# Kernel tuning notes

Measured on AMD Instinct MI355X. Metric: run time of the kernel, lower is better.

Reference implementation:

```python
import jax, jax.numpy as jnp
import numpy as np

B, C, H, W = 2, 64, 256, 256
K, DG, PAD = 3, 8, 1
KK = K * K
CG = C // DG


def _conv(x, w, b):
    y = jax.lax.conv_general_dilated(x, w, (1, 1), [(PAD, PAD), (PAD, PAD)],
                                     dimension_numbers=('NCHW', 'OIHW', 'NCHW'))
    return y + b[None, :, None, None]


def _bilinear_one(img, y, x):
    # img: (CG, H, W); y, x: (KK, H, W) float sampling coords; zero-padded bilinear
    y0 = jnp.floor(y)
    x0 = jnp.floor(x)
    wy = y - y0
    wx = x - x0

    def tap(yi, xi, wgt):
        valid = (yi >= 0) & (yi < H) & (xi >= 0) & (xi < W)
        yc = jnp.clip(yi, 0, H - 1).astype(jnp.int32)
        xc = jnp.clip(xi, 0, W - 1).astype(jnp.int32)
        v = img[:, yc, xc]  # (CG, KK, H, W)
        return v * (wgt * valid)[None]

    return (tap(y0, x0, (1 - wy) * (1 - wx)) +
            tap(y0, x0 + 1, (1 - wy) * wx) +
            tap(y0 + 1, x0, wy * (1 - wx)) +
            tap(y0 + 1, x0 + 1, wy * wx))


_sample = jax.vmap(jax.vmap(_bilinear_one))  # over batch, then deform group


def setup_inputs() -> dict:
    key = jax.random.key(0)
    ks = jax.random.split(key, 7)
    n_off = 2 * KK * DG
    n_msk = KK * DG
    bound = 1.0 / np.sqrt(C * K * K)  # kaiming_uniform(a=sqrt(5)) bound
    return {
        'ref': jax.random.normal(ks[0], (B, C, H, W), jnp.float32),
        'neighbour': jax.random.normal(ks[1], (B, C, H, W), jnp.float32),
        'off_w': jax.random.normal(ks[2], (n_off, 2 * C, K, K), jnp.float32) * 0.01,
        'off_b': jnp.zeros((n_off,), jnp.float32),
        'mask_w': jax.random.normal(ks[3], (n_msk, 2 * C, K, K), jnp.float32) * 0.01,
        'mask_b': jnp.zeros((n_msk,), jnp.float32),
        'weight': jax.random.uniform(ks[4], (C, C, K, K), jnp.float32, -bound, bound),
        'bias': jnp.zeros((C,), jnp.float32),
    }


def reference(ref, neighbour, off_w, off_b, mask_w, mask_b, weight, bias):
    concat = jnp.concatenate([ref, neighbour], axis=1)            # (B, 2C, H, W)
    offset = _conv(concat, off_w, off_b)                          # (B, 2*DG*KK, H, W)
    mask = jax.nn.sigmoid(_conv(concat, mask_w, mask_b))          # (B, DG*KK, H, W)

    off = offset.reshape(B, DG, KK, 2, H, W)
    dy, dx = off[:, :, :, 0], off[:, :, :, 1]

    ki, kj = jnp.meshgrid(jnp.arange(K), jnp.arange(K), indexing='ij')
    ki = ki.reshape(KK).astype(jnp.float32)
    kj = kj.reshape(KK).astype(jnp.float32)
    base_y = jnp.arange(H, dtype=jnp.float32)[None, :, None] - PAD + ki[:, None, None]
    base_x = jnp.arange(W, dtype=jnp.float32)[None, None, :] - PAD + kj[:, None, None]
    ys = dy + base_y                                              # (B, DG, KK, H, W)
    xs = dx + base_x

    img_g = neighbour.reshape(B, DG, CG, H, W)
    sampled = _sample(img_g, ys, xs)                              # (B, DG, CG, KK, H, W)
    sampled = sampled * mask.reshape(B, DG, 1, KK, H, W)

    wr = weight.reshape(C, DG, CG, KK)
    out = jnp.einsum('bgckhw,ogck->bohw', sampled, wr)
    return out + bias[None, :, None, None]
```

## Files before the change

kernel.cpp:

```cpp
#include <hip/hip_runtime.h>
#include <hip/hip_fp16.h>
#include <cstdint>
#include <cstddef>

#define B_ 2
#define C_ 64
#define H_ 256
#define W_ 256
#define HW_ (H_*W_)
#define DG_ 8
#define CG_ 8
#define KK_ 9
#define NOFF_ 144
#define NMSK_ 72
#define NTOT_ 216
#define KRED_ 1152
#define XPH_ 258

typedef __bf16 bf16x8 __attribute__((ext_vector_type(8)));
typedef _Float16 half8 __attribute__((ext_vector_type(8)));
typedef short  short8 __attribute__((ext_vector_type(8)));
typedef float  f32x4  __attribute__((ext_vector_type(4)));

__device__ __forceinline__ short f2bf(float f) {
    union { float f; uint32_t u; } a; a.f = f;
    uint32_t u = a.u;
    uint32_t r = (u + 0x7fffu + ((u >> 16) & 1u)) >> 16;
    return (short)r;
}

typedef __attribute__((address_space(1))) const unsigned int g_u32;
typedef __attribute__((address_space(3))) unsigned int l_u32;
__device__ __forceinline__ void gl_lds16(const void* g, void* l) {
    __builtin_amdgcn_global_load_lds((g_u32*)g, (l_u32*)l, 16, 0, 0);
}

__global__ __launch_bounds__(256) void prep_all(
    const float* __restrict__ ref, const float* __restrict__ nbr,
    const float* __restrict__ off_w, const float* __restrict__ msk_w,
    const float* __restrict__ weight,
    short* __restrict__ xp, short* __restrict__ nbf,
    short* __restrict__ Bw, short* __restrict__ Bw3)
{
    const int bid = blockIdx.x;
    const int tid = threadIdx.x;

    if (bid < 2064) {
        const int by = bid >> 2;
        const int c4 = bid & 3;
        const int b  = by / XPH_;
        const int yi = by - b * XPH_;
        const int yg = yi - 1;
        const float* base = (c4 < 2 ? ref : nbr)
                            + ((size_t)b * 64 + (c4 & 1) * 32) * HW_;
        short* rowbase = xp + (((size_t)(b * 4 + c4) * XPH_ + yi) * XPH_) * 32;
        for (int xi = tid; xi < XPH_; xi += 256) {
            const int xg = xi - 1;
            const bool valid = ((unsigned)yg < H_) && ((unsigned)xg < W_);
            short* dst = rowbase + (size_t)xi * 32;
            const int sig = (xi >> 1) & 3;
            #pragma unroll
            for (int q = 0; q < 4; ++q) {
                float v[8];
                if (valid) {
                    const float* p = base + (size_t)(q * 8) * HW_
                                     + (size_t)yg * W_ + xg;
                    #pragma unroll
                    for (int j = 0; j < 8; ++j) v[j] = p[(size_t)j * HW_];
                } else {
                    #pragma unroll
                    for (int j = 0; j < 8; ++j) v[j] = 0.f;
                }
                short8 o;
                #pragma unroll
                for (int j = 0; j < 8; ++j) o[j] = f2bf(v[j]);
                *reinterpret_cast<short8*>(dst + ((q ^ sig) * 8)) = o;
                if (c4 >= 2 && valid) {
                    const int g = (c4 - 2) * 4 + q;
                    union { half8 h8; short8 s8; } u;
                    #pragma unroll
                    for (int j = 0; j < 8; ++j) u.h8[j] = (_Float16)v[j];
                    *reinterpret_cast<short8*>(
                        nbf + ((size_t)(b * 8 + g) * HW_
                               + (size_t)yg * W_ + xg) * 8) = u.s8;
                }
            }
        }
    } else if (bid < 3216) {
        int idx = (bid - 2064) * 256 + tid;
        int s    = idx >> 13;
        int rem  = idx & 8191;
        int n    = rem >> 5;
        int slot = (rem >> 3) & 3;
        int j    = rem & 7;
        int q    = slot ^ ((n >> 1) & 3);
        int c4   = s / 9;
        int tap  = s - c4 * 9;
        int ch   = c4 * 32 + q * 8 + j;
        float v = 0.f;
        if (n < NOFF_)      v = off_w[(size_t)n * KRED_ + ch * 9 + tap];
        else if (n < NTOT_) v = msk_w[(size_t)(n - NOFF_) * KRED_ + ch * 9 + tap];
        Bw[idx] = f2bf(v);
    } else {
        int idx = (bid - 3216) * 256 + tid;
        int kc   = idx >> 11;
        int rem  = idx & 2047;
        int n    = rem >> 5;
        int slot = (rem >> 3) & 3;
        int j    = rem & 7;
        int q    = slot ^ ((n >> 1) & 3);
        int k    = kc >> 1;
        int g    = ((kc & 1) << 2) + q;
        int ci   = g * 8 + j;
        union { _Float16 h; short s; } cv;
        cv.h = (_Float16)weight[((size_t)n * 64 + ci) * 9 + k];
        Bw3[idx] = cv.s;
    }
}

struct OffV { float dy, dx, mm; };
struct GathV { half8 c00, c01, c10, c11; float a00, a01, a10, a11; };

__global__ __launch_bounds__(512, 4) void fused_conv_apply(
    const short* __restrict__ xp, const short* __restrict__ Bw,
    const float* __restrict__ off_b, const float* __restrict__ msk_b,
    const short* __restrict__ nbf, const short* __restrict__ Bw3,
    const float* __restrict__ bias, float* __restrict__ out)
{
    __shared__ __align__(16) short AsBuf[2][4608];
    __shared__ __align__(16) short offmsk[NTOT_ * 128];

    const int tid  = threadIdx.x;
    const int lane = tid & 63;
    const int wid  = tid >> 6;
    const int wm   = wid & 1;
    const int wn   = wid >> 1;
    const int col     = lane & 15;
    const int quad    = lane >> 4;
    const int rowbase = quad * 4;

    const int bid = blockIdx.x;
    const int wg  = (bid & 7) * 128 + (bid >> 3);
    const int m0 = wg << 7;
    const int b  = m0 >> 16;
    const int h  = (m0 >> 8) & 255;
    const int w0 = m0 & 255;

    {
        int bOff[4];
        #pragma unroll
        for (int nt = 0; nt < 4; ++nt) {
            int n = wn * 64 + nt * 16 + col;
            bOff[nt] = (n * 4 + (quad ^ ((n >> 1) & 3))) * 8;
        }
        int pxv[4];
        #pragma unroll
        for (int mt = 0; mt < 4; ++mt) pxv[mt] = wm * 64 + mt * 16 + col;

        f32x4 acc[4][4];
        #pragma unroll
        for (int i = 0; i < 4; ++i)
            #pragma unroll
            for (int j = 0; j < 4; ++j) acc[i][j] = f32x4{0.f, 0.f, 0.f, 0.f};

        auto stageA = [&](int win, int bb) {
            const int c4s = win / 3;
            const int dys = win - c4s * 3;
            const short* sA = xp + (((size_t)(b * 4 + c4s) * XPH_ + (h + dys)) * XPH_
                                    + w0) * 32;
            char* dA = (char*)&AsBuf[bb][0];
            gl_lds16(sA + (size_t)tid * 8, dA + wid * 1024);
            if (tid < 32) gl_lds16(sA + (size_t)(512 + tid) * 8, dA + 8192);
        };

        stageA(0, 0);
        __syncthreads();

        #pragma unroll 1
        for (int win = 0; win < 12; ++win) {
            const int bb = win & 1;
            if (win < 11) stageA(win + 1, bb ^ 1);
            const short* AsC = &AsBuf[bb][0];

            #pragma unroll
            for (int dx = 0; dx < 3; ++dx) {
                const int s = win * 3 + dx;
                const short* bp = Bw + ((size_t)s << 13);

                bf16x8 bv[4];
                #pragma unroll
                for (int nt = 0; nt < 4; ++nt)
                    bv[nt] = *reinterpret_cast<const bf16x8*>(bp + bOff[nt]);

                bf16x8 af[4];
                #pragma unroll
                for (int mt = 0; mt < 4; ++mt) {
                    const int px = pxv[mt] + dx;
                    af[mt] = *reinterpret_cast<const bf16x8*>(
                        &AsC[(px * 4 + (quad ^ ((px >> 1) & 3))) * 8]);
                }

                __builtin_amdgcn_s_setprio(1);
                #pragma unroll
                for (int mt = 0; mt < 4; ++mt)
                    #pragma unroll
                    for (int nt = 0; nt < 4; ++nt)
                        acc[mt][nt] = __builtin_amdgcn_mfma_f32_16x16x32_bf16(
                            af[mt], bv[nt], acc[mt][nt], 0, 0, 0);
                __builtin_amdgcn_s_setprio(0);
            }
            __syncthreads();
        }

        #pragma unroll
        for (int mt = 0; mt < 4; ++mt) {
            const int p4 = wm * 64 + mt * 16 + rowbase;
            #pragma unroll
            for (int nt = 0; nt < 4; ++nt) {
                const int n = wn * 64 + nt * 16 + col;
                if (n >= NTOT_) continue;
                const bool is_off = (n < NOFF_);
                const float bia = is_off ? off_b[n] : msk_b[n - NOFF_];
                union { uint2 u; __half hx[4]; } pk;
                #pragma unroll
                for (int rr = 0; rr < 4; ++rr) {
                    float v = acc[mt][nt][rr] + bia;
                    if (!is_off) v = 1.f / (1.f + __expf(-v));
                    pk.hx[rr] = __float2half(v);
                }
                const int byt = n * 256 + ((2 * p4) ^ ((n & 7) << 4));
                *(uint2*)((char*)offmsk + byt) = pk.u;
            }
        }
    }
    __syncthreads();

    {
        const int p     = tid & 127;
        const int q     = tid >> 7;
        const int w     = w0 + p;
        const int slotW = q ^ ((p >> 1) & 3);

        auto ldsOff = [&](int n, int pp) -> float {
            const int byt = n * 256 + ((2 * pp) ^ ((n & 7) << 4));
            return __half2float(*reinterpret_cast<const __half*>(
                (const char*)offmsk + byt));
        };
        auto loadOffs = [&](int kc) -> OffV {
            const int k = kc >> 1;
            const int g = ((kc & 1) << 2) + q;
            OffV o;
            o.dy = ldsOff(g * 18 + 2 * k,     p);
            o.dx = ldsOff(g * 18 + 2 * k + 1, p);
            o.mm = ldsOff(NOFF_ + g * 9 + k,  p);
            return o;
        };

        auto issueGather = [&](int kc, OffV o) -> GathV {
            const int k  = kc >> 1;
            const int g  = ((kc & 1) << 2) + q;
            const int ky = k / 3;
            const int kx = k - ky * 3;
            float ys = (float)(h - 1 + ky) + o.dy;
            float xs = (float)(w - 1 + kx) + o.dx;
            float y0f = floorf(ys), x0f = floorf(xs);
            float wy = ys - y0f, wx = xs - x0f;
            int y0 = (int)y0f, x0 = (int)x0f;
            int y1 = y0 + 1, x1 = x0 + 1;
            int yc0 = min(max(y0, 0), H_-1), yc1 = min(max(y1, 0), H_-1);
            float wy0v = (1.f - wy) * (((unsigned)y0 < H_) ? o.mm : 0.f);
            float wy1v = wy * (((unsigned)y1 < H_) ? o.mm : 0.f);
            int xb = min(max(x0, 0), W_-2);
            float wx0v = (((unsigned)x0 < W_) ? (1.f - wx) : 0.f);
            float wx1v = (((unsigned)x1 < W_) ? wx : 0.f);
            float sx0 = (x0 == xb) ? wx0v : ((x1 == xb) ? wx1v : 0.f);
            float sx1 = (x1 == xb + 1) ? wx1v : ((x0 == xb + 1) ? wx0v : 0.f);
            GathV gv;
            gv.a00 = wy0v * sx0; gv.a01 = wy0v * sx1;
            gv.a10 = wy1v * sx0; gv.a11 = wy1v * sx1;
            const short* nb = nbf + (size_t)(b * 8 + g) * HW_ * 8;
            const short* r0 = nb + ((size_t)yc0 * W_ + xb) * 8;
            const short* r1 = nb + ((size_t)yc1 * W_ + xb) * 8;
            gv.c00 = *reinterpret_cast<const half8*>(r0);
            gv.c01 = *reinterpret_cast<const half8*>(r0 + 8);
            gv.c10 = *reinterpret_cast<const half8*>(r1);
            gv.c11 = *reinterpret_cast<const half8*>(r1 + 8);
            return gv;
        };

        auto combineWrite = [&](int kc, const GathV& gv) {
            union { half8 h8; short8 s8; } u;
            #pragma unroll
            for (int c = 0; c < CG_; ++c) {
                float v = gv.a00 * (float)gv.c00[c] + gv.a01 * (float)gv.c01[c]
                        + gv.a10 * (float)gv.c10[c] + gv.a11 * (float)gv.c11[c];
                u.h8[c] = (_Float16)v;
            }
            *reinterpret_cast<short8*>(&AsBuf[kc & 1][(p * 4 + slotW) * 8]) = u.s8;
        };

        const int nB = wn * 16 + col;
        const short* bPtr = Bw3 + ((nB * 4 + (quad ^ ((nB >> 1) & 3))) << 3);

        f32x4 acc2[4];
        #pragma unroll
        for (int mt = 0; mt < 4; ++mt) acc2[mt] = f32x4{0.f, 0.f, 0.f, 0.f};

        {
            OffV o0 = loadOffs(0);
            GathV g0 = issueGather(0, o0);
            combineWrite(0, g0);
        }
        GathV GA = issueGather(1, loadOffs(1));
        GathV GB = issueGather(2, loadOffs(2));
        __syncthreads();

        auto bodyKC = [&](int kc, GathV& Gcur, GathV& Gnext) {
            const short* AsC = &AsBuf[kc & 1][0];

            half8 bv = *reinterpret_cast<const half8*>(bPtr + ((size_t)kc << 11));
            half8 af[4];
            #pragma unroll
            for (int mt = 0; mt < 4; ++mt) {
                const int px = wm * 64 + mt * 16 + col;
                af[mt] = *reinterpret_cast<const half8*>(
                    &AsC[(px * 4 + (quad ^ ((px >> 1) & 3))) * 8]);
            }

            if (kc + 1 < 18) combineWrite(kc + 1, Gcur);
            if (kc + 3 < 18) Gcur = issueGather(kc + 3, loadOffs(kc + 3));

            __builtin_amdgcn_s_setprio(1);
            #pragma unroll
            for (int mt = 0; mt < 4; ++mt)
                acc2[mt] = __builtin_amdgcn_mfma_f32_16x16x32_f16(
                    af[mt], bv, acc2[mt], 0, 0, 0);
            __builtin_amdgcn_s_setprio(0);
            __syncthreads();
            (void)Gnext;
        };

        #pragma unroll 1
        for (int kc2 = 0; kc2 < 18; kc2 += 2) {
            bodyKC(kc2,     GA, GB);
            bodyKC(kc2 + 1, GB, GA);
        }

        const int o = wn * 16 + col;
        const float bo = bias[o];
        float* op = out + ((size_t)b * C_ + o) * HW_ + (size_t)h * W_ + w0;
        #pragma unroll
        for (int mt = 0; mt < 4; ++mt) {
            const int px = wm * 64 + mt * 16 + quad * 4;
            float4 st = make_float4(acc2[mt][0] + bo, acc2[mt][1] + bo,
                                    acc2[mt][2] + bo, acc2[mt][3] + bo);
            *(float4*)(op + px) = st;
        }
    }
}

extern "C" void kernel_launch(void* const* d_in, const int* in_sizes, int n_in,
                              void* d_out, int out_size, void* d_ws, size_t ws_size,
                              hipStream_t stream) {
    const float* ref    = (const float*)d_in[0];
    const float* nbr    = (const float*)d_in[1];
    const float* off_w  = (const float*)d_in[2];
    const float* off_b  = (const float*)d_in[3];
    const float* msk_w  = (const float*)d_in[4];
    const float* msk_b  = (const float*)d_in[5];
    const float* weight = (const float*)d_in[6];
    const float* bias   = (const float*)d_in[7];
    float* out = (float*)d_out;

    const size_t sz_Bw  = (size_t)36 * 256 * 32 * 2;
    const size_t sz_xp  = (size_t)B_ * 4 * XPH_ * XPH_ * 32 * 2
                          + 16384;
    const size_t sz_Bw3 = (size_t)18 * 64 * 32 * 2;

    char* ws = (char*)d_ws;
    short* Bw  = (short*)ws;
    short* xp  = (short*)(ws + sz_Bw);
    short* Bw3 = (short*)(ws + sz_Bw + sz_xp);
    short* nbf = (short*)(ws + sz_Bw + sz_xp + sz_Bw3);

    prep_all<<<3360, 256, 0, stream>>>(ref, nbr, off_w, msk_w, weight,
                                       xp, nbf, Bw, Bw3);
    fused_conv_apply<<<1024, 512, 0, stream>>>(xp, Bw, off_b, msk_b,
                                               nbf, Bw3, bias, out);
}
```

Measured before the change: 248.2 us.

## Vectorize input repacking per row and prefetch B-fragments one step ahead

The prep kernel now assigns one block per padded row, with threads split across the four channel quarters. Each thread loads four consecutive pixels with float4 reads instead of scalar per-pixel loads, which cuts the block count and improves load coalescing. Both GEMM loops in the fused kernel now load the next step's B-operand fragments into registers before the current MFMAs issue, hiding global-load latency. The cost is more register pressure and more special-case code for row borders.

New measurement: 487.0 us. 96.2% more time.

```diff
diff --git a/kernel.cpp b/kernel.cpp
--- a/kernel.cpp
+++ b/kernel.cpp
@@ -45,28 +45,29 @@
     const int bid = blockIdx.x;
     const int tid = threadIdx.x;
 
-    if (bid < 2064) {
-        const int by = bid >> 2;
-        const int c4 = bid & 3;
-        const int b  = by / XPH_;
-        const int yi = by - b * XPH_;
+    if (bid < 516) {
+        const int b  = bid / XPH_;
+        const int yi = bid - b * XPH_;
         const int yg = yi - 1;
+        const bool rowv = ((unsigned)yg < H_);
+        const int c4 = tid >> 6;
+        const int qd = tid & 63;
         const float* base = (c4 < 2 ? ref : nbr)
-                            + ((size_t)b * 64 + (c4 & 1) * 32) * HW_;
+                            + ((size_t)b * 64 + (c4 & 1) * 32) * HW_
+                            + (size_t)(rowv ? yg : 0) * W_;
         short* rowbase = xp + (((size_t)(b * 4 + c4) * XPH_ + yi) * XPH_) * 32;
-        for (int xi = tid; xi < XPH_; xi += 256) {
+
+        auto packPix = [&](int xi) {
             const int xg = xi - 1;
-            const bool valid = ((unsigned)yg < H_) && ((unsigned)xg < W_);
+            const bool valid = rowv && ((unsigned)xg < W_);
             short* dst = rowbase + (size_t)xi * 32;
             const int sig = (xi >> 1) & 3;
             #pragma unroll
             for (int q = 0; q < 4; ++q) {
                 float v[8];
                 if (valid) {
-                    const float* p = base + (size_t)(q * 8) * HW_
-                                     + (size_t)yg * W_ + xg;
-                    #pragma unroll
-                    for (int j = 0; j < 8; ++j) v[j] = p[(size_t)j * HW_];
+                    #pragma unroll
+                    for (int j = 0; j < 8; ++j) v[j] = base[(size_t)(q*8+j) * HW_ + xg];
                 } else {
                     #pragma unroll
                     for (int j = 0; j < 8; ++j) v[j] = 0.f;
@@ -76,18 +77,52 @@
                 for (int j = 0; j < 8; ++j) o[j] = f2bf(v[j]);
                 *reinterpret_cast<short8*>(dst + ((q ^ sig) * 8)) = o;
                 if (c4 >= 2 && valid) {
-                    const int g = (c4 - 2) * 4 + q;
                     union { half8 h8; short8 s8; } u;
                     #pragma unroll
                     for (int j = 0; j < 8; ++j) u.h8[j] = (_Float16)v[j];
                     *reinterpret_cast<short8*>(
-                        nbf + ((size_t)(b * 8 + g) * HW_
+                        nbf + ((size_t)(b * 8 + (c4 - 2) * 4 + q) * HW_
                                + (size_t)yg * W_ + xg) * 8) = u.s8;
                 }
             }
-        }
-    } else if (bid < 3216) {
-        int idx = (bid - 2064) * 256 + tid;
+        };
+
+        if (rowv && qd < 63) {
+            const int xg0 = qd * 4;
+            #pragma unroll
+            for (int q = 0; q < 4; ++q) {
+                f32x4 vj[8];
+                #pragma unroll
+                for (int j = 0; j < 8; ++j)
+                    vj[j] = *reinterpret_cast<const f32x4*>(base + (size_t)(q*8+j) * HW_ + xg0);
+                #pragma unroll
+                for (int k = 0; k < 4; ++k) {
+                    const int xi = xg0 + 1 + k;
+                    const int sig = (xi >> 1) & 3;
+                    short8 o;
+                    #pragma unroll
+                    for (int j = 0; j < 8; ++j) o[j] = f2bf(vj[j][k]);
+                    *reinterpret_cast<short8*>(rowbase + (size_t)xi * 32 + ((q ^ sig) * 8)) = o;
+                    if (c4 >= 2) {
+                        union { half8 h8; short8 s8; } u;
+                        #pragma unroll
+                        for (int j = 0; j < 8; ++j) u.h8[j] = (_Float16)vj[j][k];
+                        *reinterpret_cast<short8*>(
+                            nbf + ((size_t)(b * 8 + (c4 - 2) * 4 + q) * HW_
+                                   + (size_t)yg * W_ + (xi - 1)) * 8) = u.s8;
+                    }
+                }
+            }
+        } else if (qd < 63) {
+            packPix(qd * 4 + 1); packPix(qd * 4 + 2);
+            packPix(qd * 4 + 3); packPix(qd * 4 + 4);
+        } else {
+            packPix(0);
+            packPix(253); packPix(254); packPix(255);
+            packPix(256); packPix(257);
+        }
+    } else if (bid < 1668) {
+        int idx = (bid - 516) * 256 + tid;
         int s    = idx >> 13;
         int rem  = idx & 8191;
         int n    = rem >> 5;
@@ -102,7 +137,7 @@
         else if (n < NTOT_) v = msk_w[(size_t)(n - NOFF_) * KRED_ + ch * 9 + tap];
         Bw[idx] = f2bf(v);
     } else {
-        int idx = (bid - 3216) * 256 + tid;
+        int idx = (bid - 1668) * 256 + tid;
         int kc   = idx >> 11;
         int rem  = idx & 2047;
         int n    = rem >> 5;
@@ -173,6 +208,11 @@
             if (tid < 32) gl_lds16(sA + (size_t)(512 + tid) * 8, dA + 8192);
         };
 
+        bf16x8 bvC[4];
+        #pragma unroll
+        for (int nt = 0; nt < 4; ++nt)
+            bvC[nt] = *reinterpret_cast<const bf16x8*>(Bw + bOff[nt]);
+
         stageA(0, 0);
         __syncthreads();
 
@@ -185,12 +225,14 @@
             #pragma unroll
             for (int dx = 0; dx < 3; ++dx) {
                 const int s = win * 3 + dx;
-                const short* bp = Bw + ((size_t)s << 13);
-
-                bf16x8 bv[4];
-                #pragma unroll
-                for (int nt = 0; nt < 4; ++nt)
-                    bv[nt] = *reinterpret_cast<const bf16x8*>(bp + bOff[nt]);
+
+                bf16x8 bvN[4];
+                if (s < 35) {
+                    const short* bp = Bw + ((size_t)(s + 1) << 13);
+                    #pragma unroll
+                    for (int nt = 0; nt < 4; ++nt)
+                        bvN[nt] = *reinterpret_cast<const bf16x8*>(bp + bOff[nt]);
+                }
 
                 bf16x8 af[4];
                 #pragma unroll
@@ -206,8 +248,13 @@
                     #pragma unroll
                     for (int nt = 0; nt < 4; ++nt)
                         acc[mt][nt] = __builtin_amdgcn_mfma_f32_16x16x32_bf16(
-                            af[mt], bv[nt], acc[mt][nt], 0, 0, 0);
+                            af[mt], bvC[nt], acc[mt][nt], 0, 0, 0);
                 __builtin_amdgcn_s_setprio(0);
+
+                if (s < 35) {
+                    #pragma unroll
+                    for (int nt = 0; nt < 4; ++nt) bvC[nt] = bvN[nt];
+                }
             }
             __syncthreads();
         }
@@ -313,12 +360,16 @@
         }
         GathV GA = issueGather(1, loadOffs(1));
         GathV GB = issueGather(2, loadOffs(2));
+        half8 bvC = *reinterpret_cast<const half8*>(bPtr);
         __syncthreads();
 
-        auto bodyKC = [&](int kc, GathV& Gcur, GathV& Gnext) {
+        auto bodyKC = [&](int kc, GathV& Gcur) {
             const short* AsC = &AsBuf[kc & 1][0];
 
-            half8 bv = *reinterpret_cast<const half8*>(bPtr + ((size_t)kc << 11));
+            half8 bvN;
+            if (kc + 1 < 18)
+                bvN = *reinterpret_cast<const half8*>(bPtr + ((size_t)(kc + 1) << 11));
+
             half8 af[4];
             #pragma unroll
             for (int mt = 0; mt < 4; ++mt) {
@@ -334,16 +385,16 @@
             #pragma unroll
             for (int mt = 0; mt < 4; ++mt)
                 acc2[mt] = __builtin_amdgcn_mfma_f32_16x16x32_f16(
-                    af[mt], bv, acc2[mt], 0, 0, 0);
+                    af[mt], bvC, acc2[mt], 0, 0, 0);
             __builtin_amdgcn_s_setprio(0);
             __syncthreads();
-            (void)Gnext;
+            bvC = bvN;
         };
 
         #pragma unroll 1
         for (int kc2 = 0; kc2 < 18; kc2 += 2) {
-            bodyKC(kc2,     GA, GB);
-            bodyKC(kc2 + 1, GB, GA);
+            bodyKC(kc2,     GA);
+            bodyKC(kc2 + 1, GB);
         }
 
         const int o = wn * 16 + col;
@@ -383,7 +434,7 @@
     short* Bw3 = (short*)(ws + sz_Bw + sz_xp);
     short* nbf = (short*)(ws + sz_Bw + sz_xp + sz_Bw3);
 
-    prep_all<<<3360, 256, 0, stream>>>(ref, nbr, off_w, msk_w, weight,
+    prep_all<<<1812, 256, 0, stream>>>(ref, nbr, off_w, msk_w, weight,
                                        xp, nbf, Bw, Bw3);
     fused_conv_apply<<<1024, 512, 0, stream>>>(xp, Bw, off_b, msk_b,
                                                nbf, Bw3, bias, out);
```
